# Performance work log

Measured on AMD Instinct MI355X. Metric: run time of the kernel, lower is better.

Reference implementation:

```python
import jax, jax.numpy as jnp
import numpy as np
from math import factorial

# ----- hyperparams (mirror init_kwargs) -----
HIDDEN = [(32,0,1),(32,0,-1),(8,1,1),(8,1,-1),(4,2,1),(4,2,-1)]  # (mul, l, parity)
SCALAR = [(32,0,1)]
SH_IRR = [(1,0,1),(1,1,-1),(1,2,1)]  # spherical harmonics 0e+1o+2e
EMB, NUM_RBF, R_MAX, MLP_DIM, D_IN = 32, 16, 10.0, 256, 64
N_NODES, N_EDGES, N_GRAPHS = 2048, 8192, 8
EDGE_FEATS_DIM = NUM_RBF + 2*EMB

def _slices(irs):
    s, o = [], 0
    for m, l, _ in irs:
        s.append(o); o += m*(2*l+1)
    return s

def _su2_cg(j1, j2, j3, m1, m2, m3):
    if m1 + m2 != m3:
        return 0.0
    f = factorial
    pref = ((2*j3+1)*f(j3+j1-j2)*f(j3-j1+j2)*f(j1+j2-j3)/f(j1+j2+j3+1))**0.5
    pref *= (f(j3+m3)*f(j3-m3)*f(j1-m1)*f(j1+m1)*f(j2-m2)*f(j2+m2))**0.5
    s = 0.0
    for k in range(0, j1+j2-j3+1):
        if j1-m1-k < 0 or j2+m2-k < 0 or j3-j2+m1+k < 0 or j3-j1-m2+k < 0:
            continue
        s += (-1.0)**k/(f(k)*f(j1+j2-j3-k)*f(j1-m1-k)*f(j2+m2-k)*f(j3-j2+m1+k)*f(j3-j1-m2+k))
    return pref*s

def _q(l):  # real -> complex change of basis (e3nn convention incl. (-i)^l phase)
    q = np.zeros((2*l+1, 2*l+1), dtype=np.complex128)
    for m in range(-l, 0):
        q[l+m, l+abs(m)] = 2**-0.5
        q[l+m, l-abs(m)] = -1j*2**-0.5
    q[l, l] = 1.0
    for m in range(1, l+1):
        q[l+m, l+abs(m)] = (-1)**m*2**-0.5
        q[l+m, l-abs(m)] = 1j*(-1)**m*2**-0.5
    return (-1j)**l*q

def _real_cg(l1, l2, l3):  # real-basis Clebsch-Gordan, unit Frobenius norm (wigner-3j-like)
    C = np.zeros((2*l1+1, 2*l2+1, 2*l3+1), dtype=np.complex128)
    for m1 in range(-l1, l1+1):
        for m2 in range(-l2, l2+1):
            m3 = m1 + m2
            if abs(m3) <= l3:
                C[l1+m1, l2+m2, l3+m3] = _su2_cg(l1, l2, l3, m1, m2, m3)
    w = np.einsum('ai,bj,ck,abc->ijk', _q(l1), _q(l2), np.conj(_q(l3)), C)
    re, im = np.real(w), np.imag(w)
    w = re if np.linalg.norm(re) >= np.linalg.norm(im) else im
    return (w/np.linalg.norm(w)).astype(np.float32)

_CG = {}
def cg(l1, l2, l3):
    if (l1, l2, l3) not in _CG:
        _CG[(l1, l2, l3)] = jnp.asarray(_real_cg(l1, l2, l3))
    return _CG[(l1, l2, l3)]

def _build_layer(ir_in, ir_out):  # FullyConnectedTensorProduct path enumeration
    si = _slices(ir_in)
    paths, woff, fan = [], 0, [0]*len(ir_out)
    for i1, (m1, l1, p1) in enumerate(ir_in):
        for (_, l2, p2) in SH_IRR:
            for i3, (m3, l3, p3) in enumerate(ir_out):
                if p1*p2 == p3 and abs(l1-l2) <= l3 <= l1+l2:
                    paths.append((si[i1], m1, l1, l2, i3, m3, l3, woff))
                    fan[i3] += m1
                    woff += m1*m3
    return paths, woff, fan, ir_out

L_SPECS = [_build_layer(SCALAR, HIDDEN), _build_layer(HIDDEN, HIDDEN),
           _build_layer(HIDDEN, HIDDEN), _build_layer(HIDDEN, SCALAR)]
W_NUMELS = [s[1] for s in L_SPECS]  # [1408, 4320, 4320, 1408]

def spherical_harmonics(u):  # component-normalized real SH, l=0,1,2, on unit vectors
    xc, yc, zc = u[:, 0], u[:, 1], u[:, 2]
    s3, s15, s5 = 3**0.5, 15**0.5, 5**0.5
    return jnp.stack([jnp.ones_like(xc),
                      s3*yc, s3*zc, s3*xc,
                      s15*xc*yc, s15*yc*zc, s5*0.5*(3*zc*zc-1.0), s15*xc*zc,
                      s15*0.5*(xc*xc-yc*yc)], axis=1)

def tp_messages(x, sh, w, spec):  # per-edge equivariant tensor product with edge-dep weights
    paths, _, fan, ir_out = spec
    E = x.shape[0]
    outs = [jnp.zeros((E, m*(2*l+1)), x.dtype) for m, l, _ in ir_out]
    for (o1, m1, l1, l2, i3, m3, l3, woff) in paths:
        xp = x[:, o1:o1+m1*(2*l1+1)].reshape(E, m1, 2*l1+1)
        shp = sh[:, l2*l2:(l2+1)*(l2+1)]
        wp = w[:, woff:woff+m1*m3].reshape(E, m1, m3)
        alpha = float(np.sqrt((2*l3+1)/fan[i3]))  # component/element path normalization
        y = alpha*jnp.einsum('eui,ej,euv,ijk->evk', xp, shp, wp, cg(l1, l2, l3))
        outs[i3] = outs[i3] + y.reshape(E, -1)
    return jnp.concatenate(outs, axis=1)

def batch_norm(h, ir_out, eps=1e-5):  # e3nn-style equivariant batch norm (train stats, identity affine)
    outs, o = [], 0
    for m, l, _ in ir_out:
        d = m*(2*l+1)
        f = h[:, o:o+d].reshape(-1, m, 2*l+1); o += d
        if l == 0:
            f = f - f.mean(axis=0, keepdims=True)
        norm2 = (f*f).mean(axis=(0, 2), keepdims=True)
        outs.append((f*jax.lax.rsqrt(norm2+eps)).reshape(h.shape[0], -1))
    return jnp.concatenate(outs, axis=1)

def scatter_mean(msg, idx, n):
    s = jax.ops.segment_sum(msg, idx, num_segments=n)
    c = jax.ops.segment_sum(jnp.ones((idx.shape[0], 1), msg.dtype), idx, num_segments=n)
    return s/jnp.maximum(c, 1.0)

def _forward(x, pos, edge_index, batch, emb_w, emb_b, layer_params):
    ei = jnp.concatenate([edge_index, edge_index[::-1]], axis=1)  # to_undirected (both directions)
    src, dst = ei[0], ei[1]
    h = x@emb_w + emb_b  # (N, 32)
    vec = pos[src] - pos[dst]
    lengths = jnp.linalg.norm(vec, axis=-1)
    sh = spherical_harmonics(vec/lengths[:, None])  # (E, 9)
    mu = jnp.linspace(0.0, R_MAX, NUM_RBF)
    sigma = R_MAX/NUM_RBF
    rbf = jnp.exp(-(((lengths[:, None]-mu)/sigma)**2))  # (E, 16)
    for li, (w1, b1, w2, b2) in enumerate(layer_params):
        ef = jnp.concatenate([rbf, h[src, :EMB], h[dst, :EMB]], axis=1)  # (E, 80)
        w = jax.nn.relu(ef@w1 + b1)@w2 + b2  # per-edge TP weights (dropout=eval noop)
        upd = scatter_mean(tp_messages(h[dst], sh, w, L_SPECS[li]), src, N_NODES)
        upd = batch_norm(upd, L_SPECS[li][3])
        d = upd.shape[-1]
        h_res = h[:, :d] if h.shape[-1] >= d else jnp.pad(h, ((0, 0), (0, d-h.shape[-1])))
        h = upd + h_res  # residual with pad/truncate (F.pad semantics)
    graph = jax.ops.segment_sum(h, batch, num_segments=N_GRAPHS)
    return h, graph

def setup_inputs():
    key = jax.random.key(0)
    ks = jax.random.split(key, 32)
    inp = {}
    inp['x'] = jax.random.normal(ks[0], (N_NODES, D_IN), jnp.float32)
    inp['pos'] = 3.0*jax.random.normal(ks[1], (N_NODES, 3), jnp.float32)
    s = jax.random.randint(ks[2], (N_EDGES,), 0, N_NODES)
    d = (s + jax.random.randint(ks[3], (N_EDGES,), 1, N_NODES)) % N_NODES  # no self-loops
    inp['edge_index'] = jnp.stack([s, d]).astype(jnp.int32)
    inp['batch'] = jnp.sort(jax.random.randint(ks[4], (N_NODES,), 0, N_GRAPHS)).astype(jnp.int32)
    inp['emb_w'] = jax.random.normal(ks[5], (D_IN, EMB), jnp.float32)/np.sqrt(D_IN)
    inp['emb_b'] = jnp.zeros((EMB,), jnp.float32)
    k = 6
    for i, wn in enumerate(W_NUMELS):
        inp[f'l{i}_w1'] = jax.random.normal(ks[k], (EDGE_FEATS_DIM, MLP_DIM), jnp.float32)/np.sqrt(EDGE_FEATS_DIM); k += 1
        inp[f'l{i}_b1'] = jnp.zeros((MLP_DIM,), jnp.float32)
        inp[f'l{i}_w2'] = jax.random.normal(ks[k], (MLP_DIM, wn), jnp.float32)/np.sqrt(MLP_DIM); k += 1
        inp[f'l{i}_b2'] = jnp.zeros((wn,), jnp.float32)
    return inp

def reference(x, pos, edge_index, batch, emb_w, emb_b,
              l0_w1, l0_b1, l0_w2, l0_b2, l1_w1, l1_b1, l1_w2, l1_b2,
              l2_w1, l2_b1, l2_w2, l2_b2, l3_w1, l3_b1, l3_w2, l3_b2):
    lp = [(l0_w1, l0_b1, l0_w2, l0_b2), (l1_w1, l1_b1, l1_w2, l1_b2),
          (l2_w1, l2_b1, l2_w2, l2_b2), (l3_w1, l3_b1, l3_w2, l3_b2)]
    return _forward(x, pos, edge_index, batch, emb_w, emb_b, lp)
```

## Files before the change

### kernel.cpp

```cpp
#include <hip/hip_runtime.h>
#include <hip/hip_bf16.h>
#include <math.h>

#define NNODES 2048
#define NEDG   8192
#define E2     16384
#define NGRAPH 8
#define HSTR   152

static const int LD_DIN[4]  = {32,152,152,152};
static const int LD_DOUT[4] = {152,152,152,32};
static const int LD_WN[4]   = {1408,4320,4320,1408};
static const int LD_WNP[4]  = {1408,4352,4352,1408};
static const int LD_NCH[4]  = {88,88,88,32};
static const int LD_RES[4]  = {32,152,152,152};
#define WNP_MAX 4352

#define SLOT_MAX    1088
#define CELL_N      20
#define SEG_S_N     164
#define SEG_ENT_MAX 1024

typedef short bf16x8 __attribute__((ext_vector_type(8)));
typedef float f32x4  __attribute__((ext_vector_type(4)));

constexpr double cfact(int n){ double r=1.0; for(int i=2;i<=n;i++) r*=(double)i; return r; }
constexpr double csqrt(double x){
  if(x<=0.0) return 0.0;
  double g = x>1.0? x:1.0;
  for(int i=0;i<64;i++) g=0.5*(g+x/g);
  return g;
}
constexpr double csu2cg(int j1,int j2,int j3,int m1,int m2,int m3){
  if(m1+m2!=m3) return 0.0;
  double pref = csqrt((double)(2*j3+1)*cfact(j3+j1-j2)*cfact(j3-j1+j2)*cfact(j1+j2-j3)/cfact(j1+j2+j3+1));
  pref *= csqrt(cfact(j3+m3)*cfact(j3-m3)*cfact(j1-m1)*cfact(j1+m1)*cfact(j2-m2)*cfact(j2+m2));
  double s=0.0;
  for(int k=0;k<=j1+j2-j3;k++){
    if(j1-m1-k<0||j2+m2-k<0||j3-j2+m1+k<0||j3-j1-m2+k<0) continue;
    double t=1.0/(cfact(k)*cfact(j1+j2-j3-k)*cfact(j1-m1-k)*cfact(j2+m2-k)*cfact(j3-j2+m1+k)*cfact(j3-j1-m2+k));
    s += (k&1)? -t : t;
  }
  return pref*s;
}
struct QM { double r[25]; double i[25]; };
constexpr QM cqmat(int l){
  QM q{};
  const double inv2=0.7071067811865476;
  for(int m=-l;m<0;m++){
    int am=-m;
    q.r[(l+m)*5+(l+am)] = inv2;
    q.i[(l+m)*5+(l-am)] = -inv2;
  }
  q.r[l*5+l]=1.0;
  for(int m=1;m<=l;m++){
    double sgn=(m&1)? -1.0:1.0;
    q.r[(l+m)*5+(l+m)] = sgn*inv2;
    q.i[(l+m)*5+(l-m)] = sgn*inv2;
  }
  for(int rep=0;rep<l;rep++){
    for(int t=0;t<25;t++){ double a=q.r[t], b=q.i[t]; q.r[t]=b; q.i[t]=-a; }
  }
  return q;
}
struct CGCell { float v[125]; };
constexpr CGCell mkcell(int l1,int l2,int l3){
  CGCell out{};
  int lo = l1>l2? l1-l2 : l2-l1;
  if(l3<lo || l3>l1+l2) return out;
  QM q1=cqmat(l1), q2=cqmat(l2), q3=cqmat(l3);
  int n1=2*l1+1,n2=2*l2+1,n3=2*l3+1;
  double C[125]={};
  for(int a=0;a<n1;a++)for(int b=0;b<n2;b++)for(int c=0;c<n3;c++)
    C[a*25+b*5+c]=csu2cg(l1,l2,l3,a-l1,b-l2,c-l3);
  double wr[125]={}, wi[125]={};
  for(int i=0;i<n1;i++)for(int j=0;j<n2;j++)for(int k=0;k<n3;k++){
    double ar=0.0, ai=0.0;
    for(int a=0;a<n1;a++)for(int b=0;b<n2;b++){
      double p1r=q1.r[a*5+i], p1i=q1.i[a*5+i];
      double p2r=q2.r[b*5+j], p2i=q2.i[b*5+j];
      double pr=p1r*p2r-p1i*p2i, pi=p1r*p2i+p1i*p2r;
      for(int c=0;c<n3;c++){
        double cv=C[a*25+b*5+c]; if(cv==0.0) continue;
        double p3r=q3.r[c*5+k], p3i=-q3.i[c*5+k];
        ar += (pr*p3r-pi*p3i)*cv;
        ai += (pr*p3i+pi*p3r)*cv;
      }
    }
    wr[i*25+j*5+k]=ar; wi[i*25+j*5+k]=ai;
  }
  double sr=0.0, si=0.0;
  for(int t=0;t<125;t++){ sr+=wr[t]*wr[t]; si+=wi[t]*wi[t]; }
  double nr=csqrt(sr), ni=csqrt(si);
  bool use_re = nr>=ni;
  double nn = use_re? nr:ni;
  double inv = (nn>1e-300)? 1.0/nn : 0.0;
  for(int t=0;t<125;t++) out.v[t]=(float)((use_re? wr[t]:wi[t])*inv);
  return out;
}
constexpr CGCell CGc0 =mkcell(0,0,0), CGc1 =mkcell(0,0,1), CGc2 =mkcell(0,0,2);
constexpr CGCell CGc3 =mkcell(0,1,0), CGc4 =mkcell(0,1,1), CGc5 =mkcell(0,1,2);
constexpr CGCell CGc6 =mkcell(0,2,0), CGc7 =mkcell(0,2,1), CGc8 =mkcell(0,2,2);
constexpr CGCell CGc9 =mkcell(1,0,0), CGc10=mkcell(1,0,1), CGc11=mkcell(1,0,2);
constexpr CGCell CGc12=mkcell(1,1,0), CGc13=mkcell(1,1,1), CGc14=mkcell(1,1,2);
constexpr CGCell CGc15=mkcell(1,2,0), CGc16=mkcell(1,2,1), CGc17=mkcell(1,2,2);
constexpr CGCell CGc18=mkcell(2,0,0), CGc19=mkcell(2,0,1), CGc20=mkcell(2,0,2);
constexpr CGCell CGc21=mkcell(2,1,0), CGc22=mkcell(2,1,1), CGc23=mkcell(2,1,2);
constexpr CGCell CGc24=mkcell(2,2,0), CGc25=mkcell(2,2,1), CGc26=mkcell(2,2,2);
__constant__ CGCell g_cg[27] = {
  CGc0,CGc1,CGc2,CGc3,CGc4,CGc5,CGc6,CGc7,CGc8,
  CGc9,CGc10,CGc11,CGc12,CGc13,CGc14,CGc15,CGc16,CGc17,
  CGc18,CGc19,CGc20,CGc21,CGc22,CGc23,CGc24,CGc25,CGc26};

#define IRH_INIT {{32,0,1},{32,0,-1},{8,1,1},{8,1,-1},{4,2,1},{4,2,-1}}
#define IRS_INIT {{32,0,1}}
#define SH2_INIT {{0,1},{1,-1},{2,1}}

struct PathB { int x_off,m1,d1,sh_off,d2,d3,m3,woff,out_sl,cg_idx,zbase,i3,cell; float alpha; };

__global__ __launch_bounds__(256) void build_tables_kernel(
    unsigned* __restrict__ slot_tab, unsigned* __restrict__ cell_tab,
    int* __restrict__ seg_start, unsigned* __restrict__ seg_ent,
    int* __restrict__ perm, float* __restrict__ alpha_col){
  __shared__ PathB P[32];
  __shared__ int npath_s, zcount_s, wn_s, ncell_s;
  __shared__ int cellcg[16];
  __shared__ int vals[256];
  __shared__ int part[256];
  int tid=threadIdx.x;
  int li=blockIdx.x;
  if(tid==0){
    const int IRH[6][3]=IRH_INIT;
    const int IRS[1][3]=IRS_INIT;
    const int SH2[3][2]=SH2_INIT;
    const int (*irin)[3]  = (li==0)? IRS: IRH; int nin =(li==0)?1:6;
    const int (*irout)[3] = (li==3)? IRS: IRH; int nout=(li==3)?1:6;
    int si_in[6], si_out[6];
    { int o=0; for(int i=0;i<nin;i++){ si_in[i]=o;  o+=irin[i][0]*(2*irin[i][1]+1);} }
    { int o=0; for(int i=0;i<nout;i++){ si_out[i]=o; o+=irout[i][0]*(2*irout[i][1]+1);} }
    int fan[6]={0,0,0,0,0,0};
    int np=0, woff=0, zb=0, nc=0;
    for(int i1=0;i1<nin;i1++){
      int m1=irin[i1][0], l1=irin[i1][1], p1=irin[i1][2];
      for(int s=0;s<3;s++){
        int l2=SH2[s][0], p2=SH2[s][1];
        for(int i3=0;i3<nout;i3++){
          int m3=irout[i3][0], l3=irout[i3][1], p3=irout[i3][2];
          int lo = l1>l2? l1-l2 : l2-l1;
          if(p1*p2==p3 && l3>=lo && l3<=l1+l2){
            PathB pr;
            pr.x_off=si_in[i1]; pr.m1=m1; pr.d1=2*l1+1;
            pr.sh_off=l2*l2; pr.d2=2*l2+1; pr.d3=2*l3+1;
            pr.m3=m3; pr.woff=woff; pr.out_sl=si_out[i3];
            pr.cg_idx=l1*9+l2*3+l3; pr.zbase=zb; pr.i3=i3; pr.alpha=0.f;
            int ci=-1;
            for(int c=0;c<nc;c++) if(cellcg[c]==pr.cg_idx) ci=c;
            if(ci<0){ cellcg[nc]=pr.cg_idx; ci=nc++; }
            pr.cell=ci;
            P[np++]=pr;
            fan[i3]+=m1; woff+=m1*m3; zb+=m1*(2*l3+1);
          }
        }
      }
    }
    for(int p=0;p<np;p++)
      P[p].alpha=(float)sqrt((double)(2*((P[p].d3-1)/2)+1)/(double)fan[P[p].i3]);
    npath_s=np; zcount_s=zb; wn_s=woff; ncell_s=nc;
  }
  __syncthreads();
  int np=npath_s, zc=zcount_s, nc=ncell_s, wn=wn_s;
  for(int c=tid;c<nc;c+=256){
    int cgi=cellcg[c];
    int l2=(cgi/3)%3;
    cell_tab[li*CELL_N+c]=(unsigned)cgi | ((unsigned)(l2*l2)<<8) | ((unsigned)(2*l2+1)<<12);
  }
  for(int s=tid;s<zc;s+=256){
    int p=0; while(p+1<np && P[p+1].zbase<=s) p++;
    int rel=s-P[p].zbase;
    int k=rel/P[p].m1, u=rel-k*P[p].m1;
    slot_tab[li*SLOT_MAX+s]=(unsigned)(P[p].x_off+u*P[p].d1) | ((unsigned)k<<9) | ((unsigned)P[p].cell<<12);
  }
  int* pm=perm+li*WNP_MAX;
  float* ac=alpha_col+li*WNP_MAX;
  for(int j=tid;j<wn;j+=256){
    int p=0; while(p+1<np && P[p+1].woff<=j) p++;
    int rel=j-P[p].woff;
    int v=rel/P[p].m1, u=rel%P[p].m1;
    pm[j]=P[p].woff+u*P[p].m3+v;
    ac[j]=P[p].alpha;
  }
  int Dout=(li==3)?32:152;
  for(int d=tid;d<Dout;d+=256){
    int cnt=0;
    for(int p=0;p<np;p++){
      int rel=d-P[p].out_sl;
      if(rel>=0 && rel<P[p].m3*P[p].d3) cnt++;
    }
    vals[d]=cnt;
  }
  __syncthreads();
  int v0=(tid<Dout)? vals[tid]:0;
  part[tid]=v0;
  __syncthreads();
  for(int ofs=1;ofs<256;ofs<<=1){
    int v=(tid>=ofs)? part[tid-ofs]:0;
    __syncthreads();
    part[tid]+=v;
    __syncthreads();
  }
  int* sst=seg_start+li*SEG_S_N;
  if(tid<Dout) sst[tid]=part[tid]-v0;
  if(tid==0) sst[Dout]=part[255];
  __syncthreads();
  unsigned* se=seg_ent+li*SEG_ENT_MAX;
  for(int d=tid;d<Dout;d+=256){
    int pos=sst[d];
    for(int p=0;p<np;p++){
      int rel=d-P[p].out_sl;
      if(rel>=0 && rel<P[p].m3*P[p].d3){
        int v=rel/P[p].d3, k=rel%P[p].d3;
        unsigned z0=(unsigned)(P[p].zbase+k*P[p].m1);
        unsigned w0=(unsigned)(P[p].woff+v*P[p].m1);
        unsigned code=(P[p].m1==32)?2u:((P[p].m1==8)?1u:0u);
        se[pos]= z0 | (w0<<11) | (code<<24);
        pos++;
      }
    }
  }
}

static void host_enum(int li, int& zc, int& nc){
  const int IRH[6][3]=IRH_INIT;
  const int IRS[1][3]=IRS_INIT;
  const int SH2[3][2]=SH2_INIT;
  const int (*irin)[3]  = (li==0)? IRS: IRH; int nin =(li==0)?1:6;
  const int (*irout)[3] = (li==3)? IRS: IRH; int nout=(li==3)?1:6;
  zc=0; nc=0;
  int cells[32];
  for(int i1=0;i1<nin;i1++){
    int m1=irin[i1][0], l1=irin[i1][1], p1=irin[i1][2];
    for(int s=0;s<3;s++){
      int l2=SH2[s][0], p2=SH2[s][1];
      for(int i3=0;i3<nout;i3++){
        int m3=irout[i3][0], l3=irout[i3][1], p3=irout[i3][2];
        int lo = l1>l2? l1-l2 : l2-l1;
        if(p1*p2==p3 && l3>=lo && l3<=l1+l2){
          zc+=m1*(2*l3+1);
          int cg=l1*9+l2*3+l3; int ci=-1;
          for(int c=0;c<nc;c++) if(cells[c]==cg) ci=c;
          if(ci<0) cells[nc++]=cg;
        }
      }
    }
  }
}

__global__ void geom_kernel(const float* __restrict__ pos, const int* __restrict__ ei,
                            int* __restrict__ src2, int* __restrict__ dst2,
                            float* __restrict__ sh, float* __restrict__ rbf,
                            int* __restrict__ counts){
  int e=blockIdx.x*256+threadIdx.x;
  if(e>=E2) return;
  int s,d;
  if(e<NEDG){ s=ei[e]; d=ei[NEDG+e]; }
  else { int j=e-NEDG; s=ei[NEDG+j]; d=ei[j]; }
  src2[e]=s; dst2[e]=d;
  atomicAdd(&counts[s],1);
  float vx=pos[s*3+0]-pos[d*3+0];
  float vy=pos[s*3+1]-pos[d*3+1];
  float vz=pos[s*3+2]-pos[d*3+2];
  float len=sqrtf(vx*vx+vy*vy+vz*vz);
  float inv=1.f/len;
  float x=vx*inv, y=vy*inv, z=vz*inv;
  const float s3=1.7320508075688772f, s15=3.872983346207417f, s5=2.23606797749979f;
  float* shp=sh+(size_t)e*9;
  shp[0]=1.f; shp[1]=s3*y; shp[2]=s3*z; shp[3]=s3*x;
  shp[4]=s15*x*y; shp[5]=s15*y*z; shp[6]=s5*0.5f*(3.f*z*z-1.f);
  shp[7]=s15*x*z; shp[8]=s15*0.5f*(x*x-y*y);
  float* rp=rbf+(size_t)e*16;
  const float invsig=1.6f;
  for(int k=0;k<16;k++){
    float t=(len-(10.0f/15.0f)*(float)k)*invsig;
    rp[k]=expf(-t*t);
  }
}

__global__ void scan_kernel(const int* __restrict__ counts, int* __restrict__ row_ptr){
  __shared__ int part[256];
  int t=threadIdx.x;
  int base=t*8;
  int loc[8]; int s=0;
  #pragma unroll
  for(int i=0;i<8;i++){ loc[i]=counts[base+i]; s+=loc[i]; }
  part[t]=s; __syncthreads();
  for(int ofs=1; ofs<256; ofs<<=1){
    int v=(t>=ofs)? part[t-ofs]:0;
    __syncthreads();
    part[t]+=v;
    __syncthreads();
  }
  int run=part[t]-s;
  #pragma unroll
  for(int i=0;i<8;i++){ row_ptr[base+i]=run; run+=loc[i]; }
  if(t==255) row_ptr[NNODES]=run;
}

__global__ void csr_fill_kernel(const int* __restrict__ src2, const int* __restrict__ row_ptr,
                                int* __restrict__ cursor, int* __restrict__ eidx){
  int e=blockIdx.x*256+threadIdx.x;
  if(e>=E2) return;
  int s=src2[e];
  int p=atomicAdd(&cursor[s],1);
  eidx[row_ptr[s]+p]=e;
}

__global__ void embed_kernel(const float* __restrict__ x, const float* __restrict__ W,
                             const float* __restrict__ b, float* __restrict__ h){
  int idx=blockIdx.x*256+threadIdx.x;
  int n=idx>>5, j=idx&31;
  float acc=b[j];
  for(int k=0;k<64;k++) acc += x[n*64+k]*W[k*32+j];
  h[(size_t)n*HSTR+j]=acc;
}

__global__ void cast_w2t_kernel(const float* __restrict__ w2, const int* __restrict__ perm,
                                const float* __restrict__ alpha_col,
                                __hip_bfloat16* __restrict__ w2t, int wn, int wn_pad){
  int idx=blockIdx.x*256+threadIdx.x;
  if(idx>=wn_pad*256) return;
  int j=idx>>8, k=idx&255;
  float v=(j<wn)? w2[(size_t)k*wn+perm[j]]*alpha_col[j] : 0.f;
  w2t[idx]=__float2bfloat16(v);
}

__global__ __launch_bounds__(256) void mlp1_kernel(
    const float* __restrict__ h, const float* __restrict__ rbf,
    const int* __restrict__ src2, const int* __restrict__ dst2,
    const float* __restrict__ w1, const float* __restrict__ b1,
    __hip_bfloat16* __restrict__ hidden, int e_start){
  __shared__ float ef[16][80];
  int tid=threadIdx.x;
  int e0=e_start+blockIdx.x*16;
  for(int t=tid;t<16*80;t+=256){
    int el=t/80, k=t-el*80; int ge=e0+el;
    float v;
    if(k<16)      v=rbf[(size_t)ge*16+k];
    else if(k<48) v=h[(size_t)src2[ge]*HSTR+(k-16)];
    else          v=h[(size_t)dst2[ge]*HSTR+(k-48)];
    ef[el][k]=v;
  }
  __syncthreads();
  float acc[16];
  float bv=b1[tid];
  #pragma unroll
  for(int e=0;e<16;e++) acc[e]=bv;
  for(int k=0;k<80;k++){
    float wv=w1[k*256+tid];
    #pragma unroll
    for(int e=0;e<16;e++) acc[e]+=ef[e][k]*wv;
  }
  int le0=blockIdx.x*16;
  #pragma unroll
  for(int e=0;e<16;e++)
    hidden[(size_t)(le0+e)*256+tid]=__float2bfloat16(fmaxf(acc[e],0.f));
}

__global__ __launch_bounds__(256) void mlp2_mfma_kernel(
    const __hip_bfloat16* __restrict__ hidden,
    const __hip_bfloat16* __restrict__ w2t,
    const float* __restrict__ b2, const int* __restrict__ perm,
    const float* __restrict__ alpha_col,
    __hip_bfloat16* __restrict__ wbuf, int wn, int wn_pad){
  __shared__ __hip_bfloat16 As[128*32];
  __shared__ __hip_bfloat16 Bs[128*32];
  int tid=threadIdx.x;
  int lane=tid&63;
  int m0=blockIdx.x*128, n0=blockIdx.y*128;
  int mw=((tid>>6)&1)*64, nw=(tid>>7)*64;
  f32x4 acc[4][4];
  #pragma unroll
  for(int i=0;i<4;i++)
    #pragma unroll
    for(int j=0;j<4;j++) acc[i][j]=(f32x4){0.f,0.f,0.f,0.f};

  int i0=tid*8, i1=tid*8+2048;
  int ar0=i0>>5, ac0=i0&31, ar1=i1>>5, ac1=i1&31;
  const int q4=lane>>4, c16=lane&15;

  for(int k0=0;k0<256;k0+=32){
    __syncthreads();
    *(uint4*)&As[ar0*32+ac0] = *(const uint4*)&hidden[(size_t)(m0+ar0)*256 + k0 + ac0];
    *(uint4*)&As[ar1*32+ac1] = *(const uint4*)&hidden[(size_t)(m0+ar1)*256 + k0 + ac1];
    *(uint4*)&Bs[ar0*32+ac0] = *(const uint4*)&w2t[(size_t)(n0+ar0)*256 + k0 + ac0];
    *(uint4*)&Bs[ar1*32+ac1] = *(const uint4*)&w2t[(size_t)(n0+ar1)*256 + k0 + ac1];
    __syncthreads();
    bf16x8 af[4], bfr[4];
    #pragma unroll
    for(int mi=0;mi<4;mi++) af[mi]=*(bf16x8*)&As[(mw+mi*16+c16)*32 + q4*8];
    #pragma unroll
    for(int ni=0;ni<4;ni++) bfr[ni]=*(bf16x8*)&Bs[(nw+ni*16+c16)*32 + q4*8];
    #pragma unroll
    for(int mi=0;mi<4;mi++)
      #pragma unroll
      for(int ni=0;ni<4;ni++)
        acc[mi][ni]=__builtin_amdgcn_mfma_f32_16x16x32_bf16(af[mi],bfr[ni],acc[mi][ni],0,0,0);
  }
  #pragma unroll
  for(int ni=0;ni<4;ni++){
    int col=n0+nw+ni*16+c16;
    float bias=(col<wn)? b2[perm[col]]*alpha_col[col]:0.f;
    #pragma unroll
    for(int mi=0;mi<4;mi++){
      int row=m0+mw+mi*16+q4*4;
      #pragma unroll
      for(int rr=0;rr<4;rr++)
        wbuf[(size_t)(row+rr)*wn_pad+col]=__float2bfloat16(acc[mi][ni][rr]+bias);
    }
  }
}

__device__ inline void wave_sync(){
  __builtin_amdgcn_s_waitcnt(0);
  __builtin_amdgcn_wave_barrier();
}

__device__ inline float dot8f(const float* zp, const __hip_bfloat16* wp){
  f32x4 za=*(const f32x4*)zp;
  f32x4 zb=*(const f32x4*)(zp+4);
  uint4 wv=*(const uint4*)wp;
  const __hip_bfloat16* wl=(const __hip_bfloat16*)&wv;
  float s=0.f;
  #pragma unroll
  for(int t=0;t<4;t++) s+=za[t]*__bfloat162float(wl[t]);
  #pragma unroll
  for(int t=0;t<4;t++) s+=zb[t]*__bfloat162float(wl[4+t]);
  return s;
}
__device__ inline float dot4f(const float* zp, const __hip_bfloat16* wp){
  f32x4 za=*(const f32x4*)zp;
  uint2 wv=*(const uint2*)wp;
  const __hip_bfloat16* wl=(const __hip_bfloat16*)&wv;
  float s=0.f;
  #pragma unroll
  for(int t=0;t<4;t++) s+=za[t]*__bfloat162float(wl[t]);
  return s;
}

__global__ __launch_bounds__(256) void tp4_kernel(
    const float* __restrict__ h, const float* __restrict__ sh,
    const __hip_bfloat16* __restrict__ wbuf, const int* __restrict__ dst2,
    const unsigned* __restrict__ slot_tab, const unsigned* __restrict__ cell_tab,
    const int* __restrict__ seg_start, const unsigned* __restrict__ seg_ent,
    float* __restrict__ msg, int e_start, int Din, int Dout, int wstride,
    int zc, int nc){
  __shared__ float xrow[4][160];
  __shared__ float shs[4][12];
  __shared__ float zsm[4][1088];
  __shared__ float Tw[4][376];
  int tid=threadIdx.x, w=tid>>6, lane=tid&63;
  int le=blockIdx.x*4+w, ge=e_start+le;
  int dn=dst2[ge];
  for(int i=lane;i<Din;i+=64) xrow[w][i]=h[(size_t)dn*HSTR+i];
  for(int i=Din+lane;i<160;i+=64) xrow[w][i]=0.f;
  if(lane<9) shs[w][lane]=sh[(size_t)ge*9+lane];
  wave_sync();
  float* T=&Tw[w][0];
  for(int t=lane;t<nc*25;t+=64){
    int c=t/25, r=t-c*25, k=r/5, i=r-k*5;
    unsigned cm=cell_tab[c];
    int cgi=cm&255, sho=(cm>>8)&15, d2=(cm>>12)&7;
    const float* cgp=g_cg[cgi].v + i*25 + k;
    float s=0.f;
    for(int j=0;j<d2;j++) s+=cgp[j*5]*shs[w][sho+j];
    T[t]=s;
  }
  wave_sync();
  const float* xr=&xrow[w][0];
  for(int s=lane;s<zc;s+=64){
    unsigned st=slot_tab[s];
    int xb=st&511, k=(st>>9)&7, c=st>>12;
    const float* Tp=&T[c*25+k*5];
    zsm[w][s]=xr[xb]*Tp[0]+xr[xb+1]*Tp[1]+xr[xb+2]*Tp[2]+xr[xb+3]*Tp[3]+xr[xb+4]*Tp[4];
  }
  wave_sync();
  const __hip_bfloat16* wrow=wbuf+(size_t)le*wstride;
  const float* zbase=&zsm[w][0];
  for(int d=lane;d<Dout;d+=64){
    int s0=seg_start[d], s1=seg_start[d+1];
    float acc=0.f;
    for(int s=s0;s<s1;s++){
      unsigned sg=seg_ent[s];
      int z0=sg&2047, w0=(sg>>11)&8191, code=sg>>24;
      const float* zp=zbase+z0;
      const __hip_bfloat16* wp=wrow+w0;
      if(code==2){
        #pragma unroll
        for(int t=0;t<4;t++) acc+=dot8f(zp+t*8,wp+t*8);
      } else if(code==1){
        acc+=dot8f(zp,wp);
      } else {
        acc+=dot4f(zp,wp);
      }
    }
    msg[(size_t)ge*Dout+d]=acc;
  }
}

__global__ void aggregate_kernel(const float* __restrict__ msg, const int* __restrict__ row_ptr,
                                 const int* __restrict__ eidx, const int* __restrict__ counts,
                                 float* __restrict__ upd, int Dout){
  int n=blockIdx.x; int lane=threadIdx.x;
  int p0=row_ptr[n], p1=row_ptr[n+1];
  int c=counts[n]; if(c<1) c=1;
  float inv=1.f/(float)c;
  for(int d=lane;d<Dout;d+=64){
    float s=0.f;
    for(int p=p0;p<p1;p++) s+=msg[(size_t)eidx[p]*Dout+d];
    upd[(size_t)n*Dout+d]=s*inv;
  }
}

__device__ inline int hidden_chan_of_dim(int d){
  if(d<64)  return d;
  if(d<88)  return 64+(d-64)/3;
  if(d<112) return 72+(d-88)/3;
  if(d<132) return 80+(d-112)/5;
  return 84+(d-132)/5;
}
__device__ inline void hidden_chan_params(int c, int& off, int& dk, int& l0){
  if(c<64){ off=c; dk=1; l0=1; }
  else if(c<72){ off=64+(c-64)*3; dk=3; l0=0; }
  else if(c<80){ off=88+(c-72)*3; dk=3; l0=0; }
  else if(c<84){ off=112+(c-80)*5; dk=5; l0=0; }
  else { off=132+(c-84)*5; dk=5; l0=0; }
}

__global__ void stats_kernel(const float* __restrict__ upd, float* __restrict__ stats,
                             int Dout, int scalar_out){
  int c=blockIdx.x, tid=threadIdx.x;
  int off,dk,l0;
  if(scalar_out){ off=c; dk=1; l0=1; }
  else hidden_chan_params(c,off,dk,l0);
  float s=0.f, s2=0.f;
  int total=NNODES*dk;
  for(int t=tid;t<total;t+=256){
    int n=t/dk, k=t-n*dk;
    float v=upd[(size_t)n*Dout+off+k];
    s+=v; s2+=v*v;
  }
  __shared__ float rs[256], rs2[256];
  rs[tid]=s; rs2[tid]=s2; __syncthreads();
  for(int o=128;o>0;o>>=1){
    if(tid<o){ rs[tid]+=rs[tid+o]; rs2[tid]+=rs2[tid+o]; }
    __syncthreads();
  }
  if(tid==0){
    float cnt=(float)total;
    float mean = l0? rs[0]/cnt : 0.f;
    float var = rs2[0]/cnt - mean*mean;
    stats[c*2]=mean;
    stats[c*2+1]=1.0f/sqrtf(var+1e-5f);
  }
}

__global__ void apply_kernel(const float* __restrict__ upd, const float* __restrict__ stats,
                             const float* __restrict__ h_cur, float* __restrict__ h_next,
                             int Dout, int res_dim, int scalar_out, int out_stride){
  int idx=blockIdx.x*256+threadIdx.x;
  if(idx>=NNODES*Dout) return;
  int n=idx/Dout, d=idx-n*Dout;
  int c = scalar_out? d : hidden_chan_of_dim(d);
  float v=(upd[idx]-stats[2*c])*stats[2*c+1];
  float res=(d<res_dim)? h_cur[(size_t)n*HSTR+d] : 0.f;
  h_next[(size_t)n*out_stride+d]=v+res;
}

__global__ void graph_kernel(const float* __restrict__ hfin, const int* __restrict__ batch,
                             float* __restrict__ gout){
  int idx=blockIdx.x*256+threadIdx.x;
  int n=idx>>5, d=idx&31;
  atomicAdd(&gout[batch[n]*32+d], hfin[idx]);
}

extern "C" void kernel_launch(void* const* d_in, const int* in_sizes, int n_in,
                              void* d_out, int out_size, void* d_ws, size_t ws_size,
                              hipStream_t stream){
  (void)in_sizes; (void)n_in; (void)out_size;
  const float* x    =(const float*)d_in[0];
  const float* pos  =(const float*)d_in[1];
  const int*   ei   =(const int*)d_in[2];
  const int*   batch=(const int*)d_in[3];
  const float* emb_w=(const float*)d_in[4];
  const float* emb_b=(const float*)d_in[5];
  const float *W1[4], *B1[4], *W2[4], *B2[4];
  for(int l=0;l<4;l++){
    W1[l]=(const float*)d_in[6+4*l];
    B1[l]=(const float*)d_in[7+4*l];
    W2[l]=(const float*)d_in[8+4*l];
    B2[l]=(const float*)d_in[9+4*l];
  }
  int ZC[4], NC[4];
  for(int l=0;l<4;l++) host_enum(l,ZC[l],NC[l]);

  char* base=(char*)d_ws;
  size_t off=0;
  auto alloc=[&](size_t bytes)->char*{
    off=(off+255)&~(size_t)255;
    char* p=base+off; off+=bytes; return p;
  };
  float*  h_a   =(float*)alloc((size_t)NNODES*HSTR*4);
  float*  h_b   =(float*)alloc((size_t)NNODES*HSTR*4);
  float*  shb   =(float*)alloc((size_t)E2*9*4);
  float*  rbfb  =(float*)alloc((size_t)E2*16*4);
  int*    src2  =(int*)  alloc((size_t)E2*4);
  int*    dst2  =(int*)  alloc((size_t)E2*4);
  int*    counts=(int*)  alloc((size_t)NNODES*4);
  int*    cursor=(int*)  alloc((size_t)NNODES*4);
  int*    row_ptr=(int*) alloc((size_t)(NNODES+4)*4);
  int*    eidx  =(int*)  alloc((size_t)E2*4);
  float*  msg   =(float*)alloc((size_t)E2*HSTR*4);
  float*  upd   =(float*)alloc((size_t)NNODES*HSTR*4);
  float*  stats =(float*)alloc(256*4);
  unsigned* slot_tab=(unsigned*)alloc((size_t)4*SLOT_MAX*4);
  unsigned* cell_tg =(unsigned*)alloc((size_t)4*CELL_N*4);
  int*      seg_s   =(int*)     alloc((size_t)4*SEG_S_N*4);
  unsigned* seg_e   =(unsigned*)alloc((size_t)4*SEG_ENT_MAX*4);
  int*      perm    =(int*)     alloc((size_t)4*WNP_MAX*4);
  float*    alpha_c =(float*)   alloc((size_t)4*WNP_MAX*4);
  __hip_bfloat16* w2t[4];
  for(int l=0;l<4;l++) w2t[l]=(__hip_bfloat16*)alloc((size_t)LD_WNP[l]*256*2);

  int E_CHUNK=E2;
  while(E_CHUNK>128){
    size_t need=off;
    need=(need+255)&~(size_t)255; need+=(size_t)E_CHUNK*256*2;
    need=(need+255)&~(size_t)255; need+=(size_t)E_CHUNK*WNP_MAX*2;
    if(need<=ws_size) break;
    E_CHUNK>>=1;
  }
  __hip_bfloat16* hidden=(__hip_bfloat16*)alloc((size_t)E_CHUNK*256*2);
  __hip_bfloat16* wbuf  =(__hip_bfloat16*)alloc((size_t)E_CHUNK*WNP_MAX*2);

  hipMemsetAsync(counts,0,(size_t)NNODES*4,stream);
  hipMemsetAsync(cursor,0,(size_t)NNODES*4,stream);
  build_tables_kernel<<<4,256,0,stream>>>(slot_tab,cell_tg,seg_s,seg_e,perm,alpha_c);
  geom_kernel<<<E2/256,256,0,stream>>>(pos,ei,src2,dst2,shb,rbfb,counts);
  scan_kernel<<<1,256,0,stream>>>(counts,row_ptr);
  csr_fill_kernel<<<E2/256,256,0,stream>>>(src2,row_ptr,cursor,eidx);
  embed_kernel<<<(NNODES*32)/256,256,0,stream>>>(x,emb_w,emb_b,h_a);
  for(int l=0;l<4;l++)
    cast_w2t_kernel<<<(LD_WNP[l]*256+255)/256,256,0,stream>>>(
        W2[l],perm+l*WNP_MAX,alpha_c+l*WNP_MAX,w2t[l],LD_WN[l],LD_WNP[l]);

  float* h_cur=h_a; float* h_nxt=h_b;
  for(int li=0;li<4;li++){
    int wn=LD_WN[li], wnp=LD_WNP[li], Din=LD_DIN[li], Dout=LD_DOUT[li];
    for(int e0=0;e0<E2;e0+=E_CHUNK){
      mlp1_kernel<<<E_CHUNK/16,256,0,stream>>>(h_cur,rbfb,src2,dst2,W1[li],B1[li],hidden,e0);
      dim3 g2(E_CHUNK/128, wnp/128);
      mlp2_mfma_kernel<<<g2,256,0,stream>>>(hidden,w2t[li],B2[li],perm+li*WNP_MAX,
                                            alpha_c+li*WNP_MAX,wbuf,wn,wnp);
      tp4_kernel<<<E_CHUNK/4,256,0,stream>>>(h_cur,shb,wbuf,dst2,
          slot_tab+li*SLOT_MAX, cell_tg+li*CELL_N,
          seg_s+li*SEG_S_N, seg_e+li*SEG_ENT_MAX,
          msg,e0,Din,Dout,wnp, ZC[li], NC[li]);
    }
    aggregate_kernel<<<NNODES,64,0,stream>>>(msg,row_ptr,eidx,counts,upd,Dout);
    stats_kernel<<<LD_NCH[li],256,0,stream>>>(upd,stats,Dout,li==3?1:0);
    int tot=NNODES*Dout;
    if(li<3)
      apply_kernel<<<(tot+255)/256,256,0,stream>>>(upd,stats,h_cur,h_nxt,Dout,LD_RES[li],0,HSTR);
    else
      apply_kernel<<<(tot+255)/256,256,0,stream>>>(upd,stats,h_cur,(float*)d_out,Dout,LD_RES[li],1,32);
    float* tmp=h_cur; h_cur=h_nxt; h_nxt=tmp;
  }

  float* gout=(float*)d_out + (size_t)NNODES*32;
  hipMemsetAsync(gout,0,(size_t)NGRAPH*32*4,stream);
  graph_kernel<<<(NNODES*32)/256,256,0,stream>>>((const float*)d_out,batch,gout);
}
```

Before: 836.5 us.

## Stage per-edge TP weights in LDS and build layer specs at compile time

The tensor-product kernel now copies each edge's bf16 weight row from global memory into shared memory with vectorized loads before the dot products, instead of reading scattered global addresses inside the segment loop. Blocks shrink from four waves to two, which keeps shared memory per block roughly in check now that weight rows are added. Path enumeration moves into a constexpr LayerSpec held in constant memory, replacing the single-thread setup in the table-build kernel and the host enumeration. The extra shared memory per edge may lower occupancy, and the constexpr sqrt helper (csqrt) must exist elsewhere in the file.

New measurement: 895.3 us. +7.0%, slower.

```diff
diff --git a/kernel.cpp b/kernel.cpp
--- a/kernel.cpp
+++ b/kernel.cpp
@@ -112,89 +112,93 @@
   CGc9,CGc10,CGc11,CGc12,CGc13,CGc14,CGc15,CGc16,CGc17,
   CGc18,CGc19,CGc20,CGc21,CGc22,CGc23,CGc24,CGc25,CGc26};
 
-#define IRH_INIT {{32,0,1},{32,0,-1},{8,1,1},{8,1,-1},{4,2,1},{4,2,-1}}
-#define IRS_INIT {{32,0,1}}
-#define SH2_INIT {{0,1},{1,-1},{2,1}}
-
-struct PathB { int x_off,m1,d1,sh_off,d2,d3,m3,woff,out_sl,cg_idx,zbase,i3,cell; float alpha; };
+#define MAXP 32
+struct LayerSpec {
+  int np, zc, wn, nc;
+  int x_off[MAXP], m1[MAXP], d1[MAXP], sh_off[MAXP], d2[MAXP], d3[MAXP],
+      m3[MAXP], woff[MAXP], out_sl[MAXP], cg_idx[MAXP], zbase[MAXP], cell[MAXP];
+  float alpha[MAXP];
+  int cellcg[16];
+};
+constexpr LayerSpec mkspec(int li){
+  LayerSpec S{};
+  const int IRH[6][3]={{32,0,1},{32,0,-1},{8,1,1},{8,1,-1},{4,2,1},{4,2,-1}};
+  const int IRS[1][3]={{32,0,1}};
+  const int SH2[3][2]={{0,1},{1,-1},{2,1}};
+  const int (*irin)[3]  = (li==0)? IRS: IRH; int nin =(li==0)?1:6;
+  const int (*irout)[3] = (li==3)? IRS: IRH; int nout=(li==3)?1:6;
+  int si_in[6]={}, si_out[6]={};
+  { int o=0; for(int i=0;i<nin;i++){ si_in[i]=o;  o+=irin[i][0]*(2*irin[i][1]+1);} }
+  { int o=0; for(int i=0;i<nout;i++){ si_out[i]=o; o+=irout[i][0]*(2*irout[i][1]+1);} }
+  int fan[6]={};
+  int i3a[MAXP]={};
+  int np=0, woff=0, zb=0, nc=0;
+  for(int i1=0;i1<nin;i1++){
+    int m1=irin[i1][0], l1=irin[i1][1], p1=irin[i1][2];
+    for(int s=0;s<3;s++){
+      int l2=SH2[s][0], p2=SH2[s][1];
+      for(int i3=0;i3<nout;i3++){
+        int m3=irout[i3][0], l3=irout[i3][1], p3=irout[i3][2];
+        int lo = l1>l2? l1-l2 : l2-l1;
+        if(p1*p2==p3 && l3>=lo && l3<=l1+l2){
+          S.x_off[np]=si_in[i1]; S.m1[np]=m1; S.d1[np]=2*l1+1;
+          S.sh_off[np]=l2*l2; S.d2[np]=2*l2+1; S.d3[np]=2*l3+1;
+          S.m3[np]=m3; S.woff[np]=woff; S.out_sl[np]=si_out[i3];
+          S.cg_idx[np]=l1*9+l2*3+l3; S.zbase[np]=zb;
+          int ci=-1;
+          for(int c=0;c<nc;c++) if(S.cellcg[c]==S.cg_idx[np]) ci=c;
+          if(ci<0){ S.cellcg[nc]=S.cg_idx[np]; ci=nc++; }
+          S.cell[np]=ci; i3a[np]=i3;
+          np++;
+          fan[i3]+=m1; woff+=m1*m3; zb+=m1*(2*l3+1);
+        }
+      }
+    }
+  }
+  for(int p=0;p<np;p++)
+    S.alpha[p]=(float)csqrt((double)(2*((S.d3[p]-1)/2)+1)/(double)fan[i3a[p]]);
+  S.np=np; S.zc=zb; S.wn=woff; S.nc=nc;
+  return S;
+}
+constexpr LayerSpec LS0=mkspec(0), LS1=mkspec(1), LS2=mkspec(2), LS3=mkspec(3);
+__constant__ LayerSpec g_spec[4]={LS0,LS1,LS2,LS3};
 
 __global__ __launch_bounds__(256) void build_tables_kernel(
     unsigned* __restrict__ slot_tab, unsigned* __restrict__ cell_tab,
     int* __restrict__ seg_start, unsigned* __restrict__ seg_ent,
     int* __restrict__ perm, float* __restrict__ alpha_col){
-  __shared__ PathB P[32];
-  __shared__ int npath_s, zcount_s, wn_s, ncell_s;
-  __shared__ int cellcg[16];
   __shared__ int vals[256];
   __shared__ int part[256];
   int tid=threadIdx.x;
   int li=blockIdx.x;
-  if(tid==0){
-    const int IRH[6][3]=IRH_INIT;
-    const int IRS[1][3]=IRS_INIT;
-    const int SH2[3][2]=SH2_INIT;
-    const int (*irin)[3]  = (li==0)? IRS: IRH; int nin =(li==0)?1:6;
-    const int (*irout)[3] = (li==3)? IRS: IRH; int nout=(li==3)?1:6;
-    int si_in[6], si_out[6];
-    { int o=0; for(int i=0;i<nin;i++){ si_in[i]=o;  o+=irin[i][0]*(2*irin[i][1]+1);} }
-    { int o=0; for(int i=0;i<nout;i++){ si_out[i]=o; o+=irout[i][0]*(2*irout[i][1]+1);} }
-    int fan[6]={0,0,0,0,0,0};
-    int np=0, woff=0, zb=0, nc=0;
-    for(int i1=0;i1<nin;i1++){
-      int m1=irin[i1][0], l1=irin[i1][1], p1=irin[i1][2];
-      for(int s=0;s<3;s++){
-        int l2=SH2[s][0], p2=SH2[s][1];
-        for(int i3=0;i3<nout;i3++){
-          int m3=irout[i3][0], l3=irout[i3][1], p3=irout[i3][2];
-          int lo = l1>l2? l1-l2 : l2-l1;
-          if(p1*p2==p3 && l3>=lo && l3<=l1+l2){
-            PathB pr;
-            pr.x_off=si_in[i1]; pr.m1=m1; pr.d1=2*l1+1;
-            pr.sh_off=l2*l2; pr.d2=2*l2+1; pr.d3=2*l3+1;
-            pr.m3=m3; pr.woff=woff; pr.out_sl=si_out[i3];
-            pr.cg_idx=l1*9+l2*3+l3; pr.zbase=zb; pr.i3=i3; pr.alpha=0.f;
-            int ci=-1;
-            for(int c=0;c<nc;c++) if(cellcg[c]==pr.cg_idx) ci=c;
-            if(ci<0){ cellcg[nc]=pr.cg_idx; ci=nc++; }
-            pr.cell=ci;
-            P[np++]=pr;
-            fan[i3]+=m1; woff+=m1*m3; zb+=m1*(2*l3+1);
-          }
-        }
-      }
-    }
-    for(int p=0;p<np;p++)
-      P[p].alpha=(float)sqrt((double)(2*((P[p].d3-1)/2)+1)/(double)fan[P[p].i3]);
-    npath_s=np; zcount_s=zb; wn_s=woff; ncell_s=nc;
-  }
-  __syncthreads();
-  int np=npath_s, zc=zcount_s, nc=ncell_s, wn=wn_s;
+  const LayerSpec& S=g_spec[li];
+  int np=S.np, zc=S.zc, nc=S.nc, wn=S.wn;
   for(int c=tid;c<nc;c+=256){
-    int cgi=cellcg[c];
+    int cgi=S.cellcg[c];
     int l2=(cgi/3)%3;
     cell_tab[li*CELL_N+c]=(unsigned)cgi | ((unsigned)(l2*l2)<<8) | ((unsigned)(2*l2+1)<<12);
   }
   for(int s=tid;s<zc;s+=256){
-    int p=0; while(p+1<np && P[p+1].zbase<=s) p++;
-    int rel=s-P[p].zbase;
-    int k=rel/P[p].m1, u=rel-k*P[p].m1;
-    slot_tab[li*SLOT_MAX+s]=(unsigned)(P[p].x_off+u*P[p].d1) | ((unsigned)k<<9) | ((unsigned)P[p].cell<<12);
+    int p=0; while(p+1<np && S.zbase[p+1]<=s) p++;
+    int rel=s-S.zbase[p];
+    int k=rel/S.m1[p], u=rel-k*S.m1[p];
+    slot_tab[li*SLOT_MAX+s]=(unsigned)(S.x_off[p]+u*S.d1[p]) | ((unsigned)k<<9) | ((unsigned)S.cell[p]<<12);
   }
   int* pm=perm+li*WNP_MAX;
   float* ac=alpha_col+li*WNP_MAX;
   for(int j=tid;j<wn;j+=256){
-    int p=0; while(p+1<np && P[p+1].woff<=j) p++;
-    int rel=j-P[p].woff;
-    int v=rel/P[p].m1, u=rel%P[p].m1;
-    pm[j]=P[p].woff+u*P[p].m3+v;
-    ac[j]=P[p].alpha;
+    int p=0; while(p+1<np && S.woff[p+1]<=j) p++;
+    int rel=j-S.woff[p];
+    int v=rel/S.m1[p], u=rel%S.m1[p];
+    pm[j]=S.woff[p]+u*S.m3[p]+v;
+    ac[j]=S.alpha[p];
   }
   int Dout=(li==3)?32:152;
   for(int d=tid;d<Dout;d+=256){
     int cnt=0;
     for(int p=0;p<np;p++){
-      int rel=d-P[p].out_sl;
-      if(rel>=0 && rel<P[p].m3*P[p].d3) cnt++;
+      int rel=d-S.out_sl[p];
+      if(rel>=0 && rel<S.m3[p]*S.d3[p]) cnt++;
     }
     vals[d]=cnt;
   }
@@ -216,40 +220,14 @@
   for(int d=tid;d<Dout;d+=256){
     int pos=sst[d];
     for(int p=0;p<np;p++){
-      int rel=d-P[p].out_sl;
-      if(rel>=0 && rel<P[p].m3*P[p].d3){
-        int v=rel/P[p].d3, k=rel%P[p].d3;
-        unsigned z0=(unsigned)(P[p].zbase+k*P[p].m1);
-        unsigned w0=(unsigned)(P[p].woff+v*P[p].m1);
-        unsigned code=(P[p].m1==32)?2u:((P[p].m1==8)?1u:0u);
+      int rel=d-S.out_sl[p];
+      if(rel>=0 && rel<S.m3[p]*S.d3[p]){
+        int v=rel/S.d3[p], k=rel%S.d3[p];
+        unsigned z0=(unsigned)(S.zbase[p]+k*S.m1[p]);
+        unsigned w0=(unsigned)(S.woff[p]+v*S.m1[p]);
+        unsigned code=(S.m1[p]==32)?2u:((S.m1[p]==8)?1u:0u);
         se[pos]= z0 | (w0<<11) | (code<<24);
         pos++;
-      }
-    }
-  }
-}
-
-static void host_enum(int li, int& zc, int& nc){
-  const int IRH[6][3]=IRH_INIT;
-  const int IRS[1][3]=IRS_INIT;
-  const int SH2[3][2]=SH2_INIT;
-  const int (*irin)[3]  = (li==0)? IRS: IRH; int nin =(li==0)?1:6;
-  const int (*irout)[3] = (li==3)? IRS: IRH; int nout=(li==3)?1:6;
-  zc=0; nc=0;
-  int cells[32];
-  for(int i1=0;i1<nin;i1++){
-    int m1=irin[i1][0], l1=irin[i1][1], p1=irin[i1][2];
-    for(int s=0;s<3;s++){
-      int l2=SH2[s][0], p2=SH2[s][1];
-      for(int i3=0;i3<nout;i3++){
-        int m3=irout[i3][0], l3=irout[i3][1], p3=irout[i3][2];
-        int lo = l1>l2? l1-l2 : l2-l1;
-        if(p1*p2==p3 && l3>=lo && l3<=l1+l2){
-          zc+=m1*(2*l3+1);
-          int cg=l1*9+l2*3+l3; int ci=-1;
-          for(int c=0;c<nc;c++) if(cells[c]==cg) ci=c;
-          if(ci<0) cells[nc++]=cg;
-        }
       }
     }
   }
@@ -424,7 +402,7 @@
   __builtin_amdgcn_wave_barrier();
 }
 
-__device__ inline float dot8f(const float* zp, const __hip_bfloat16* wp){
+__device__ inline float dot8l(const float* zp, const __hip_bfloat16* wp){
   f32x4 za=*(const f32x4*)zp;
   f32x4 zb=*(const f32x4*)(zp+4);
   uint4 wv=*(const uint4*)wp;
@@ -436,7 +414,7 @@
   for(int t=0;t<4;t++) s+=zb[t]*__bfloat162float(wl[4+t]);
   return s;
 }
-__device__ inline float dot4f(const float* zp, const __hip_bfloat16* wp){
+__device__ inline float dot4l(const float* zp, const __hip_bfloat16* wp){
   f32x4 za=*(const f32x4*)zp;
   uint2 wv=*(const uint2*)wp;
   const __hip_bfloat16* wl=(const __hip_bfloat16*)&wv;
@@ -446,20 +424,24 @@
   return s;
 }
 
-__global__ __launch_bounds__(256) void tp4_kernel(
+__global__ __launch_bounds__(128) void tp5_kernel(
     const float* __restrict__ h, const float* __restrict__ sh,
     const __hip_bfloat16* __restrict__ wbuf, const int* __restrict__ dst2,
     const unsigned* __restrict__ slot_tab, const unsigned* __restrict__ cell_tab,
     const int* __restrict__ seg_start, const unsigned* __restrict__ seg_ent,
     float* __restrict__ msg, int e_start, int Din, int Dout, int wstride,
     int zc, int nc){
-  __shared__ float xrow[4][160];
-  __shared__ float shs[4][12];
-  __shared__ float zsm[4][1088];
-  __shared__ float Tw[4][376];
+  __shared__ float xrow[2][160];
+  __shared__ float shs[2][12];
+  __shared__ float zsm[2][1088];
+  __shared__ float Tw[2][376];
+  __shared__ __hip_bfloat16 wlds[2][WNP_MAX];
   int tid=threadIdx.x, w=tid>>6, lane=tid&63;
-  int le=blockIdx.x*4+w, ge=e_start+le;
+  int le=blockIdx.x*2+w, ge=e_start+le;
   int dn=dst2[ge];
+  const __hip_bfloat16* wrow=wbuf+(size_t)le*wstride;
+  for(int t=lane;t<(wstride>>3);t+=64)
+    *(uint4*)&wlds[w][t*8] = *(const uint4*)&wrow[(size_t)t*8];
   for(int i=lane;i<Din;i+=64) xrow[w][i]=h[(size_t)dn*HSTR+i];
   for(int i=Din+lane;i<160;i+=64) xrow[w][i]=0.f;
   if(lane<9) shs[w][lane]=sh[(size_t)ge*9+lane];
@@ -483,7 +465,7 @@
     zsm[w][s]=xr[xb]*Tp[0]+xr[xb+1]*Tp[1]+xr[xb+2]*Tp[2]+xr[xb+3]*Tp[3]+xr[xb+4]*Tp[4];
   }
   wave_sync();
-  const __hip_bfloat16* wrow=wbuf+(size_t)le*wstride;
+  const __hip_bfloat16* wl=&wlds[w][0];
   const float* zbase=&zsm[w][0];
   for(int d=lane;d<Dout;d+=64){
     int s0=seg_start[d], s1=seg_start[d+1];
@@ -492,14 +474,14 @@
       unsigned sg=seg_ent[s];
       int z0=sg&2047, w0=(sg>>11)&8191, code=sg>>24;
       const float* zp=zbase+z0;
-      const __hip_bfloat16* wp=wrow+w0;
+      const __hip_bfloat16* wp=wl+w0;
       if(code==2){
         #pragma unroll
-        for(int t=0;t<4;t++) acc+=dot8f(zp+t*8,wp+t*8);
+        for(int t=0;t<4;t++) acc+=dot8l(zp+t*8,wp+t*8);
       } else if(code==1){
-        acc+=dot8f(zp,wp);
+        acc+=dot8l(zp,wp);
       } else {
-        acc+=dot4f(zp,wp);
+        acc+=dot4l(zp,wp);
       }
     }
     msg[(size_t)ge*Dout+d]=acc;
@@ -599,8 +581,8 @@
     W2[l]=(const float*)d_in[8+4*l];
     B2[l]=(const float*)d_in[9+4*l];
   }
-  int ZC[4], NC[4];
-  for(int l=0;l<4;l++) host_enum(l,ZC[l],NC[l]);
+  int ZC[4]={LS0.zc,LS1.zc,LS2.zc,LS3.zc};
+  int NC[4]={LS0.nc,LS1.nc,LS2.nc,LS3.nc};
 
   char* base=(char*)d_ws;
   size_t off=0;
@@ -660,7 +642,7 @@
       dim3 g2(E_CHUNK/128, wnp/128);
       mlp2_mfma_kernel<<<g2,256,0,stream>>>(hidden,w2t[li],B2[li],perm+li*WNP_MAX,
                                             alpha_c+li*WNP_MAX,wbuf,wn,wnp);
-      tp4_kernel<<<E_CHUNK/4,256,0,stream>>>(h_cur,shb,wbuf,dst2,
+      tp5_kernel<<<E_CHUNK/2,128,0,stream>>>(h_cur,shb,wbuf,dst2,
           slot_tab+li*SLOT_MAX, cell_tg+li*CELL_N,
           seg_s+li*SEG_S_N, seg_e+li*SEG_ENT_MAX,
           msg,e0,Din,Dout,wnp, ZC[li], NC[li]);
```
